# Kernel optimization log

Hardware: AMD Instinct MI355X
Metric: run time of the kernel (lower is better)

Reference implementation:

```python
import jax, jax.numpy as jnp
import numpy as np

N = 100000; D = 256; ATT = 512; H = 8; HD = ATT // H; E = 250000
TYPE_CT = 64; TS = 64; P = 8192; PC = 1024; MP = 131072; MC = 16384


def setup_inputs() -> dict:
    key = jax.random.key(0)
    ks = jax.random.split(key, 24)
    sD = 1.0 / np.sqrt(D); sT = 1.0 / np.sqrt(TS); sA = 1.0 / np.sqrt(ATT); sC = 1.0 / np.sqrt(D + ATT)
    inp = {}
    inp['node_states'] = jax.random.normal(ks[0], (N, D), jnp.float32)
    inp['node_types'] = jax.random.randint(ks[1], (N,), 0, TYPE_CT, jnp.int32)
    inp['pair_conj'] = jax.random.randint(ks[2], (E,), 0, N, jnp.int32)
    inp['pair_prem'] = jax.random.randint(ks[3], (E,), 0, N, jnp.int32)
    inp['pool_prem_nodes'] = jax.random.randint(ks[4], (MP,), 0, N, jnp.int32)
    inp['pool_prem_seg'] = ((jnp.arange(MP, dtype=jnp.int32) * P) // MP).astype(jnp.int32)  # every prem set non-empty
    inp['pool_conj_nodes'] = jax.random.randint(ks[5], (MC,), 0, N, jnp.int32)
    inp['pool_conj_seg'] = ((jnp.arange(MC, dtype=jnp.int32) * PC) // MC).astype(jnp.int32)
    inp['prem2conj'] = jax.random.randint(ks[6], (P,), 0, PC, jnp.int32)
    # learned parameters
    inp['ln_g'] = jnp.ones((D,), jnp.float32)
    inp['ln_b'] = jnp.zeros((D,), jnp.float32)
    inp['emb_p'] = jax.random.normal(ks[7], (TYPE_CT, TS), jnp.float32) * 0.02
    inp['wp_w'] = jax.random.normal(ks[8], (TS, ATT), jnp.float32) * sT
    inp['wp_b'] = jnp.zeros((ATT,), jnp.float32)
    inp['emb_c'] = jax.random.normal(ks[9], (TYPE_CT, TS), jnp.float32) * 0.02
    inp['wc_w'] = jax.random.normal(ks[10], (TS, ATT), jnp.float32) * sT
    inp['wc_b'] = jnp.zeros((ATT,), jnp.float32)
    inp['Wq_p'] = jax.random.normal(ks[11], (H, D, HD), jnp.float32) * sD
    inp['Wk_p'] = jax.random.normal(ks[12], (H, D, HD), jnp.float32) * sD
    inp['Wv_p'] = jax.random.normal(ks[13], (H, D, HD), jnp.float32) * sD
    inp['Wo_p'] = jax.random.normal(ks[14], (ATT, ATT), jnp.float32) * sA
    inp['Wq_c'] = jax.random.normal(ks[15], (H, D, HD), jnp.float32) * sD
    inp['Wk_c'] = jax.random.normal(ks[16], (H, D, HD), jnp.float32) * sD
    inp['Wv_c'] = jax.random.normal(ks[17], (H, D, HD), jnp.float32) * sD
    inp['Wo_c'] = jax.random.normal(ks[18], (ATT, ATT), jnp.float32) * sA
    inp['W_dag'] = jax.random.normal(ks[19], (D + ATT, D + ATT), jnp.float32) * sC
    inp['b_dag'] = jnp.zeros((D + ATT,), jnp.float32)
    return inp


def _layernorm(x, g, b):
    mu = jnp.mean(x, axis=-1, keepdims=True)
    var = jnp.mean(jnp.square(x - mu), axis=-1, keepdims=True)
    return (x - mu) * jax.lax.rsqrt(var + 1e-5) * g + b


def _mha_dir(x, src, tgt, Wq, Wk, Wv, Wo, gate):
    # gather query/key/value node reprs along the pair list (irregular gather)
    xs = x[src]; xt = x[tgt]                       # [E, D]
    q = jnp.einsum('ed,hdk->ehk', xs, Wq)          # [E, H, HD]
    k = jnp.einsum('ed,hdk->ehk', xt, Wk)
    scores = jnp.sum(q * k, axis=-1) / np.sqrt(HD)  # [E, H]
    # per-query-node (segment) softmax, as in compute_att_aggr grouping
    m = jax.ops.segment_max(scores, src, num_segments=N)
    ex = jnp.exp(scores - m[src])
    denom = jax.ops.segment_sum(ex, src, num_segments=N)
    prob = ex / denom[src]
    v = jnp.einsum('ed,hdk->ehk', xt, Wv)
    # adj_matr @ comb_matr scatter-aggregation
    agg = jax.ops.segment_sum(prob[..., None] * v, src, num_segments=N)  # [N, H, HD]
    return gate * (agg.reshape(N, H * HD) @ Wo)


def reference(node_states, node_types, pair_conj, pair_prem, pool_prem_nodes, pool_prem_seg,
              pool_conj_nodes, pool_conj_seg, prem2conj,
              ln_g, ln_b, emb_p, wp_w, wp_b, emb_c, wc_w, wc_b,
              Wq_p, Wk_p, Wv_p, Wo_p, Wq_c, Wk_c, Wv_c, Wo_c, W_dag, b_dag):
    x = _layernorm(node_states, ln_g, ln_b)                                  # ne_norm(node reprs)
    gate_p = jax.nn.sigmoid(emb_p[node_types] @ wp_w + wp_b)                 # prem_gate  [N, ATT]
    gate_c = jax.nn.sigmoid(emb_c[node_types] @ wc_w + wc_b)                 # conj_gate
    # just_prem pairs: (prem, conj) -> query/scatter node = prem, key/value node = conj
    comb = _mha_dir(x, pair_prem, pair_conj, Wq_p, Wk_p, Wv_p, Wo_p, gate_p)
    # just_conj pairs: (conj, prem)
    comb = comb + _mha_dir(x, pair_conj, pair_prem, Wq_c, Wk_c, Wv_c, Wo_c, gate_c)
    h = jnp.concatenate([x, comb], axis=1)                                   # [N, D+ATT]
    pooled = jnp.tanh(h @ W_dag + b_dag)                                     # simplified dag_lstm pass
    prem_r = jax.ops.segment_max(pooled[pool_prem_nodes], pool_prem_seg, num_segments=P)
    conj_sets = jax.ops.segment_max(pooled[pool_conj_nodes], pool_conj_seg, num_segments=PC)
    conj_r = conj_sets[prem2conj]
    return jnp.concatenate([prem_r, conj_r], axis=1)                         # [P, 2*(D+ATT)]
```

## Files before the change

### kernel.cpp

```cpp
#include <hip/hip_runtime.h>
#include <math.h>

#define N_NODES 100000
#define DIM 256
#define ATT 512
#define NH 8
#define HD 64
#define E_PAIRS 250000
#define TYPE_CT 64
#define TS 64
#define P_SEG 8192
#define PC_SEG 1024
#define MP_SZ 131072
#define MC_SZ 16384
#define CD 768

typedef unsigned short u16;
typedef __attribute__((ext_vector_type(8))) short short8v;
typedef __attribute__((ext_vector_type(4))) float floatx4;

__device__ __forceinline__ u16 f2b(float f) {
    unsigned u = __float_as_uint(f);
    return (u16)((u + 0x7FFFu + ((u >> 16) & 1u)) >> 16);
}
__device__ __forceinline__ float b2f(u16 h) {
    return __uint_as_float(((unsigned)h) << 16);
}

template<int N>
__device__ __forceinline__ void waitcnt_vm() {
    asm volatile("s_waitcnt vmcnt(%0)" :: "n"(N) : "memory");
}
__device__ __forceinline__ void barrier_fence() {
    asm volatile("s_barrier" ::: "memory");
    __builtin_amdgcn_sched_barrier(0);
}

__device__ __forceinline__ void remap8(int flat, int gx, int& bx, int& by) {
    int yc = flat & 7;
    int t = flat >> 3;
    bx = t % gx;
    by = yc + 8 * (t / gx);
}

__global__ __launch_bounds__(256) void fill_val_k(float* out, int n, float v) {
    int i = blockIdx.x * 256 + threadIdx.x;
    if (i < n) out[i] = v;
}

__global__ __launch_bounds__(64) void layernorm_k(
    const float* __restrict__ ns, const float* __restrict__ g,
    const float* __restrict__ b, u16* __restrict__ x)
{
    int row = blockIdx.x;
    int lane = threadIdx.x;
    float4 v = ((const float4*)(ns + (size_t)row * DIM))[lane];
    float sum = v.x + v.y + v.z + v.w;
    #pragma unroll
    for (int off = 32; off >= 1; off >>= 1) sum += __shfl_xor(sum, off);
    float mu = sum * (1.0f / DIM);
    float dx = v.x - mu, dy = v.y - mu, dz = v.z - mu, dw = v.w - mu;
    float sq = dx * dx + dy * dy + dz * dz + dw * dw;
    #pragma unroll
    for (int off = 32; off >= 1; off >>= 1) sq += __shfl_xor(sq, off);
    float rs = rsqrtf(sq * (1.0f / DIM) + 1e-5f);
    float4 gg = ((const float4*)g)[lane];
    float4 bb = ((const float4*)b)[lane];
    u16 o4[4];
    o4[0] = f2b(dx * rs * gg.x + bb.x);
    o4[1] = f2b(dy * rs * gg.y + bb.y);
    o4[2] = f2b(dz * rs * gg.z + bb.z);
    o4[3] = f2b(dw * rs * gg.w + bb.w);
    *(uint2*)(x + (size_t)row * DIM + lane * 4) = *(uint2*)o4;
}

__global__ __launch_bounds__(512) void gate_table_k(
    const float* __restrict__ emb, const float* __restrict__ w,
    const float* __restrict__ wb, float* __restrict__ tab)
{
    int t = blockIdx.x;
    int a = threadIdx.x;
    float acc = wb[a];
    #pragma unroll 8
    for (int s = 0; s < TS; ++s) acc += emb[t * TS + s] * w[s * ATT + a];
    tab[t * ATT + a] = 1.0f / (1.0f + expf(-acc));
}

__global__ __launch_bounds__(256) void wcvt_k(
    const float* __restrict__ W, u16* __restrict__ Bt, int K, int N)
{
    int idx = blockIdx.x * 256 + threadIdx.x;
    if (idx >= K * N) return;
    int c = idx / K, k = idx - c * K;
    Bt[idx] = f2b(W[(size_t)k * N + c]);
}

__global__ __launch_bounds__(256) void wqkv_cvt_k(
    const float* __restrict__ Wq, const float* __restrict__ Wk,
    const float* __restrict__ Wv, u16* __restrict__ outp)
{
    int idx = blockIdx.x * 256 + threadIdx.x;
    if (idx >= NH * 3 * HD * DIM) return;
    int k = idx & (DIM - 1);
    int c = (idx >> 8) & (HD - 1);
    int hm = idx >> 14;
    int m = hm % 3;
    int h = hm / 3;
    const float* W = (m == 0) ? Wq : ((m == 1) ? Wk : Wv);
    outp[idx] = f2b(W[((size_t)h * DIM + k) * HD + c]);
}

template<int BM, int WN, int DEPTH, int EPI>
__device__ __forceinline__ void gemm_body3(
    int bm, int bn,
    const u16* __restrict__ A, int lda,
    const u16* __restrict__ A2, int lda2, int K1,
    const u16* __restrict__ Bt, int ldb,
    u16* __restrict__ C, int ldc,
    int M, int K,
    const float* __restrict__ bias,
    const float* __restrict__ gateTab,
    const int* __restrict__ types)
{
    constexpr int BN = 32 * WN;
    constexpr int AR = BM / 64;
    constexpr int BR = BN / 64;
    constexpr int LA = AR + BR;
    constexpr int AF = BM / 32;
    __shared__ u16 As[DEPTH][BM * 32];
    __shared__ u16 Bs[DEPTH][BN * 32];
    const int tid = threadIdx.x;
    const int wave = tid >> 6, lane = tid & 63;
    const int wm = (wave >> 1) * (BM / 2), wn = (wave & 1) * 16 * WN;
    const int srow = tid >> 2;
    const int skk = (((tid & 3) ^ ((srow >> 1) & 3)) * 8);
    floatx4 acc[AF][WN] = {};

    auto stage = [&](int buf, int k0) {
        #pragma unroll
        for (int rnd = 0; rnd < AR; ++rnd) {
            int grow = bm + srow + rnd * 64;
            if (grow > M - 1) grow = M - 1;
            int gk = k0 + skk;
            const u16* src;
            if (EPI == 2 && gk >= K1) src = A2 + (size_t)grow * lda2 + (gk - K1);
            else                      src = A + (size_t)grow * lda + gk;
            __builtin_amdgcn_global_load_lds(
                (const __attribute__((address_space(1))) void*)src,
                (__attribute__((address_space(3))) void*)(&As[buf][rnd * 2048 + wave * 512]),
                16, 0, 0);
        }
        #pragma unroll
        for (int rnd = 0; rnd < BR; ++rnd) {
            const u16* src = Bt + (size_t)(bn + srow + rnd * 64) * ldb + k0 + skk;
            __builtin_amdgcn_global_load_lds(
                (const __attribute__((address_space(1))) void*)src,
                (__attribute__((address_space(3))) void*)(&Bs[buf][rnd * 2048 + wave * 512]),
                16, 0, 0);
        }
    };

    const int NS = K >> 5;
    #pragma unroll
    for (int p = 0; p < DEPTH - 1; ++p)
        if (p < NS) stage(p, p * 32);
    const int rr = lane & 15;
    const int cq = lane >> 4;
    int cur = 0;
    for (int is = 0; is < NS; ++is) {
        int pend = NS - 1 - is;
        if (pend > DEPTH - 2) pend = DEPTH - 2;
        if (pend >= 2)      waitcnt_vm<2 * LA>();
        else if (pend == 1) waitcnt_vm<LA>();
        else                waitcnt_vm<0>();
        barrier_fence();
        if (is + DEPTH - 1 < NS) stage((cur + DEPTH - 1) % DEPTH, (is + DEPTH - 1) * 32);
        short8v a[AF], b[WN];
        #pragma unroll
        for (int i = 0; i < AF; ++i) {
            int ar = wm + i * 16 + rr;
            a[i] = *(const short8v*)&As[cur][ar * 32 + ((cq ^ ((ar >> 1) & 3)) * 8)];
        }
        #pragma unroll
        for (int j = 0; j < WN; ++j) {
            int br = wn + j * 16 + rr;
            b[j] = *(const short8v*)&Bs[cur][br * 32 + ((cq ^ ((br >> 1) & 3)) * 8)];
        }
        #pragma unroll
        for (int i = 0; i < AF; ++i)
            #pragma unroll
            for (int j = 0; j < WN; ++j)
                acc[i][j] = __builtin_amdgcn_mfma_f32_16x16x32_bf16(
                    a[i], b[j], acc[i][j], 0, 0, 0);
        cur = (cur + 1) % DEPTH;
    }
    #pragma unroll
    for (int i = 0; i < AF; ++i) {
        #pragma unroll
        for (int j = 0; j < WN; ++j) {
            #pragma unroll
            for (int q = 0; q < 4; ++q) {
                int row = bm + wm + i * 16 + (lane >> 4) * 4 + q;
                if (row >= M) continue;
                int col = bn + wn + j * 16 + (lane & 15);
                float v = acc[i][j][q];
                size_t idx = (size_t)row * ldc + col;
                if (EPI == 0) C[idx] = f2b(v);
                else if (EPI == 1) {
                    float g = gateTab[types[row] * ATT + col];
                    C[idx] = f2b(b2f(C[idx]) + g * v);
                } else if (EPI == 3) {
                    float g = gateTab[types[row] * ATT + col];
                    C[idx] = f2b(g * v);
                } else {
                    C[idx] = f2b(tanhf(v + bias[col]));
                }
            }
        }
    }
}

#define MB64 1563
#define MB64P 1568

__global__ __launch_bounds__(256) void gemm_qkv(
    const u16* __restrict__ A, const u16* __restrict__ Bt, u16* __restrict__ C)
{
    gemm_body3<64, 6, 3, 0>(blockIdx.y * 64, 0,
                            A, DIM, nullptr, 0, 1 << 30, Bt, DIM, C, 192,
                            N_NODES, DIM, nullptr, nullptr, nullptr);
}
__global__ __launch_bounds__(256) void gemm_qkv_all(
    const u16* __restrict__ A, const u16* __restrict__ Bt, u16* __restrict__ C,
    int gx)
{
    int bx, by; remap8(blockIdx.x, gx, bx, by);
    if (by >= MB64) return;
    gemm_body3<64, 6, 3, 0>(by * 64, bx * 192,
                            A, DIM, nullptr, 0, 1 << 30, Bt, DIM, C, gx * 192,
                            N_NODES, DIM, nullptr, nullptr, nullptr);
}
__global__ __launch_bounds__(256) void gemm_wo_first(
    const u16* __restrict__ A, const u16* __restrict__ Bt, u16* __restrict__ C,
    const float* __restrict__ gateTab, const int* __restrict__ types)
{
    int bx, by; remap8(blockIdx.x, 4, bx, by);
    if (by >= MB64) return;
    gemm_body3<64, 4, 3, 3>(by * 64, bx * 128,
                            A, ATT, nullptr, 0, 1 << 30, Bt, ATT, C, ATT,
                            N_NODES, ATT, nullptr, gateTab, types);
}
__global__ __launch_bounds__(256) void gemm_wo_acc(
    const u16* __restrict__ A, const u16* __restrict__ Bt, u16* __restrict__ C,
    const float* __restrict__ gateTab, const int* __restrict__ types)
{
    int bx, by; remap8(blockIdx.x, 4, bx, by);
    if (by >= MB64) return;
    gemm_body3<64, 4, 3, 1>(by * 64, bx * 128,
                            A, ATT, nullptr, 0, 1 << 30, Bt, ATT, C, ATT,
                            N_NODES, ATT, nullptr, gateTab, types);
}
__global__ __launch_bounds__(256) void gemm_dag(
    const u16* __restrict__ A, const u16* __restrict__ A2,
    const u16* __restrict__ Bt, u16* __restrict__ C,
    const float* __restrict__ bias)
{
    int bx, by; remap8(blockIdx.x, 3, bx, by);
    if (by >= MB64) return;
    gemm_body3<64, 4, 3, 2>(by * 64, bx * 128,
                            A, DIM, A2, ATT, DIM, Bt, CD, C, 384,
                            N_NODES, CD, bias, nullptr, nullptr);
}

__global__ __launch_bounds__(256) void count_k(
    const int* __restrict__ src, int* __restrict__ counts)
{
    int e = blockIdx.x * 256 + threadIdx.x;
    if (e < E_PAIRS) atomicAdd(&counts[src[e]], 1);
}
__global__ __launch_bounds__(256) void scan1_k(
    const int* __restrict__ counts, int* __restrict__ offs, int* __restrict__ bsums)
{
    __shared__ int sm[256];
    int i = blockIdx.x * 256 + threadIdx.x;
    int v = (i < N_NODES) ? counts[i] : 0;
    sm[threadIdx.x] = v;
    __syncthreads();
    for (int d = 1; d < 256; d <<= 1) {
        int t = (threadIdx.x >= d) ? sm[threadIdx.x - d] : 0;
        __syncthreads();
        sm[threadIdx.x] += t;
        __syncthreads();
    }
    if (i < N_NODES) offs[i] = sm[threadIdx.x] - v;
    if (threadIdx.x == 255) bsums[blockIdx.x] = sm[255];
}
__global__ __launch_bounds__(512) void scan2_k(int* __restrict__ bsums, int nb)
{
    __shared__ int sm[512];
    int tx = threadIdx.x;
    int v = (tx < nb) ? bsums[tx] : 0;
    sm[tx] = v;
    __syncthreads();
    for (int d = 1; d < 512; d <<= 1) {
        int t = (tx >= d) ? sm[tx - d] : 0;
        __syncthreads();
        sm[tx] += t;
        __syncthreads();
    }
    if (tx < nb) bsums[tx] = sm[tx] - v;
}
__global__ __launch_bounds__(256) void addcur_k(
    int* __restrict__ offs, const int* __restrict__ bsums, int* __restrict__ cur)
{
    int i = blockIdx.x * 256 + threadIdx.x;
    if (i >= N_NODES) return;
    int o = offs[i] + bsums[i >> 8];
    offs[i] = o;
    cur[i] = o;
}
__global__ __launch_bounds__(256) void scatter_k(
    const int* __restrict__ src, const int* __restrict__ tgt,
    int* __restrict__ cur, int* __restrict__ csr_tgt)
{
    int e = blockIdx.x * 256 + threadIdx.x;
    if (e >= E_PAIRS) return;
    int p = atomicAdd(&cur[src[e]], 1);
    csr_tgt[p] = tgt[e];
}

template<int MULTI>
__global__ __launch_bounds__(256) void attn_k(
    const u16* __restrict__ qkv, int ld,
    const int* __restrict__ offs, const int* __restrict__ counts,
    const int* __restrict__ csr_tgt, u16* __restrict__ agg, int h_in)
{
    int s = blockIdx.x * 4 + (threadIdx.x >> 6);
    if (s >= N_NODES) return;
    int hy = MULTI ? blockIdx.y : 0;
    int h = h_in + hy;
    const u16* base = qkv + hy * 192;
    int lane = threadIdx.x & 63;
    float q = b2f(base[(size_t)s * ld + lane]) * 0.125f;
    int lo = offs[s], deg = counts[s];
    float m = -INFINITY, l = 0.0f, acc = 0.0f;
    if (deg > 0) {
        int t0 = csr_tgt[lo];
        u16 kc = base[(size_t)t0 * ld + 64 + lane];
        u16 vc = base[(size_t)t0 * ld + 128 + lane];
        for (int i = 0; i < deg; ++i) {
            u16 kn = 0, vn = 0;
            if (i + 1 < deg) {
                int tn = csr_tgt[lo + i + 1];
                kn = base[(size_t)tn * ld + 64 + lane];
                vn = base[(size_t)tn * ld + 128 + lane];
            }
            float p = q * b2f(kc);
            #pragma unroll
            for (int off = 32; off >= 1; off >>= 1) p += __shfl_xor(p, off);
            float mn = fmaxf(m, p);
            float sc = expf(m - mn);
            float w  = expf(p - mn);
            l = l * sc + w;
            acc = acc * sc + w * b2f(vc);
            m = mn;
            kc = kn; vc = vn;
        }
    }
    float r = (deg > 0) ? acc / l : 0.0f;
    agg[(size_t)s * ATT + h * HD + lane] = f2b(r);
}

template<int BFOUT>
__global__ __launch_bounds__(256) void seg_max_k(
    const u16* __restrict__ pooled, const int* __restrict__ nodes,
    const int* __restrict__ seg, int total, void* __restrict__ outv, int ldo)
{
    int p = blockIdx.x;
    int lo, hi;
    { int a = 0, b2 = total; while (a < b2) { int mid = (a + b2) >> 1; if (seg[mid] < p) a = mid + 1; else b2 = mid; } lo = a; }
    { int a = lo, b2 = total; while (a < b2) { int mid = (a + b2) >> 1; if (seg[mid] < p + 1) a = mid + 1; else b2 = mid; } hi = a; }
    for (int c = threadIdx.x; c < 384; c += 256) {
        float mx = -INFINITY;
        for (int i = lo; i < hi; ++i)
            mx = fmaxf(mx, b2f(pooled[(size_t)nodes[i] * 384 + c]));
        if (BFOUT) ((u16*)outv)[(size_t)p * ldo + c] = f2b(mx);
        else       ((float*)outv)[(size_t)p * ldo + c] = mx;
    }
}

__global__ __launch_bounds__(768) void gather_conj(
    const u16* __restrict__ cs, const int* __restrict__ p2c,
    float* __restrict__ out)
{
    int p = blockIdx.x;
    int c = threadIdx.x;
    out[(size_t)p * (2 * CD) + CD + c] = b2f(cs[(size_t)p2c[p] * CD + c]);
}

extern "C" void kernel_launch(void* const* d_in, const int* in_sizes, int n_in,
                              void* d_out, int out_size, void* d_ws, size_t ws_size,
                              hipStream_t stream) {
    const float* node_states     = (const float*)d_in[0];
    const int*   node_types      = (const int*)d_in[1];
    const int*   pair_conj       = (const int*)d_in[2];
    const int*   pair_prem       = (const int*)d_in[3];
    const int*   pool_prem_nodes = (const int*)d_in[4];
    const int*   pool_prem_seg   = (const int*)d_in[5];
    const int*   pool_conj_nodes = (const int*)d_in[6];
    const int*   pool_conj_seg   = (const int*)d_in[7];
    const int*   prem2conj       = (const int*)d_in[8];
    const float* ln_g  = (const float*)d_in[9];
    const float* ln_b  = (const float*)d_in[10];
    const float* emb_p = (const float*)d_in[11];
    const float* wp_w  = (const float*)d_in[12];
    const float* wp_b  = (const float*)d_in[13];
    const float* emb_c = (const float*)d_in[14];
    const float* wc_w  = (const float*)d_in[15];
    const float* wc_b  = (const float*)d_in[16];
    const float* Wq_p  = (const float*)d_in[17];
    const float* Wk_p  = (const float*)d_in[18];
    const float* Wv_p  = (const float*)d_in[19];
    const float* Wo_p  = (const float*)d_in[20];
    const float* Wq_c  = (const float*)d_in[21];
    const float* Wk_c  = (const float*)d_in[22];
    const float* Wv_c  = (const float*)d_in[23];
    const float* Wo_c  = (const float*)d_in[24];
    const float* W_dag = (const float*)d_in[25];
    const float* b_dag = (const float*)d_in[26];
    float* out = (float*)d_out;

    char* ws = (char*)d_ws;
    size_t o = 0;
    u16* x_bf  = (u16*)(ws + o); o += (size_t)N_NODES * DIM * 2;
    u16* comb  = (u16*)(ws + o); o += (size_t)N_NODES * ATT * 2;
    u16* R     = (u16*)(ws + o); o += (size_t)N_NODES * ATT * 2;
    char* csrb = ws + o;         o += 8000000;
    u16* conj_sets = (u16*)(ws + o); o += (size_t)PC_SEG * CD * 2;
    const size_t WS_NEEDED = o;

    if (ws_size < WS_NEEDED) {
        fill_val_k<<<(out_size + 255) / 256, 256, 0, stream>>>(out, out_size, (float)ws_size);
        return;
    }
    u16* qkv_all = (u16*)(ws + WS_NEEDED);
    int batch = 1;
    if (ws_size >= WS_NEEDED + (size_t)N_NODES * 1536 * 2)      batch = 8;
    else if (ws_size >= WS_NEEDED + (size_t)N_NODES * 768 * 2)  batch = 4;
    else if (ws_size >= WS_NEEDED + (size_t)N_NODES * 384 * 2)  batch = 2;

    u16* agg    = R;
    u16* pooled = R;
    int* c_counts[2], *c_offs[2], *c_cur[2], *c_tgt[2];
    for (int d = 0; d < 2; ++d) {
        char* base = csrb + (size_t)d * 2200000;
        c_counts[d] = (int*)(base + 0);
        c_offs[d]   = (int*)(base + 400000);
        c_cur[d]    = (int*)(base + 800000);
        c_tgt[d]    = (int*)(base + 1200000);
    }
    int* bsums = (int*)(csrb + 4400000);
    u16* wdag_t = (u16*)csrb;

    char* ob = (char*)d_out;
    u16* qkv     = (u16*)(ob + 0);
    float* gtab_p = (float*)(ob + 38400000);
    float* gtab_c = (float*)(ob + 38531072);
    u16* wqkv_t  = (u16*)(ob + 38662144);
    u16* wo_t    = (u16*)(ob + 40235008);

    layernorm_k<<<N_NODES, 64, 0, stream>>>(node_states, ln_g, ln_b, x_bf);
    gate_table_k<<<TYPE_CT, ATT, 0, stream>>>(emb_p, wp_w, wp_b, gtab_p);
    gate_table_k<<<TYPE_CT, ATT, 0, stream>>>(emb_c, wc_w, wc_b, gtab_c);
    wqkv_cvt_k<<<(NH * 3 * HD * DIM + 255) / 256, 256, 0, stream>>>(
        Wq_p, Wk_p, Wv_p, wqkv_t);
    wqkv_cvt_k<<<(NH * 3 * HD * DIM + 255) / 256, 256, 0, stream>>>(
        Wq_c, Wk_c, Wv_c, wqkv_t + (size_t)NH * 3 * HD * DIM);
    wcvt_k<<<(ATT * ATT + 255) / 256, 256, 0, stream>>>(Wo_p, wo_t, ATT, ATT);
    wcvt_k<<<(ATT * ATT + 255) / 256, 256, 0, stream>>>(
        Wo_c, wo_t + (size_t)ATT * ATT, ATT, ATT);

    const int NSCAN = (N_NODES + 255) / 256;
    for (int d = 0; d < 2; ++d) {
        const int* src = d ? pair_conj : pair_prem;
        const int* tgt = d ? pair_prem : pair_conj;
        hipMemsetAsync(c_counts[d], 0, 400000, stream);
        count_k<<<(E_PAIRS + 255) / 256, 256, 0, stream>>>(src, c_counts[d]);
        scan1_k<<<NSCAN, 256, 0, stream>>>(c_counts[d], c_offs[d], bsums);
        scan2_k<<<1, 512, 0, stream>>>(bsums, NSCAN);
        addcur_k<<<NSCAN, 256, 0, stream>>>(c_offs[d], bsums, c_cur[d]);
        scatter_k<<<(E_PAIRS + 255) / 256, 256, 0, stream>>>(src, tgt, c_cur[d], c_tgt[d]);
    }

    for (int dir = 0; dir < 2; ++dir) {
        const float* gt = dir ? gtab_c : gtab_p;
        const u16* wq_d = wqkv_t + (size_t)dir * NH * 3 * HD * DIM;
        const u16* wo_d = wo_t + (size_t)dir * ATT * ATT;

        if (batch > 1) {
            for (int hb = 0; hb < NH; hb += batch) {
                gemm_qkv_all<<<batch * MB64P, 256, 0, stream>>>(
                    x_bf, wq_d + (size_t)hb * 3 * HD * DIM, qkv_all, batch);
                attn_k<1><<<dim3((N_NODES + 3) / 4, batch), 256, 0, stream>>>(
                    qkv_all, batch * 192, c_offs[dir], c_counts[dir],
                    c_tgt[dir], agg, hb);
            }
        } else {
            for (int h = 0; h < NH; ++h) {
                gemm_qkv<<<dim3(1, MB64), 256, 0, stream>>>(
                    x_bf, wq_d + (size_t)h * 3 * HD * DIM, qkv);
                attn_k<0><<<(N_NODES + 3) / 4, 256, 0, stream>>>(
                    qkv, 192, c_offs[dir], c_counts[dir], c_tgt[dir], agg, h);
            }
        }

        if (dir == 0)
            gemm_wo_first<<<4 * MB64P, 256, 0, stream>>>(
                agg, wo_d, comb, gt, node_types);
        else
            gemm_wo_acc<<<4 * MB64P, 256, 0, stream>>>(
                agg, wo_d, comb, gt, node_types);
    }

    wcvt_k<<<(CD * CD + 255) / 256, 256, 0, stream>>>(W_dag, wdag_t, CD, CD);

    for (int c0 = 0; c0 < CD; c0 += 384) {
        gemm_dag<<<3 * MB64P, 256, 0, stream>>>(
            x_bf, comb, wdag_t + (size_t)c0 * CD, pooled, b_dag + c0);
        seg_max_k<0><<<P_SEG, 256, 0, stream>>>(
            pooled, pool_prem_nodes, pool_prem_seg, MP_SZ, out + c0, 2 * CD);
        seg_max_k<1><<<PC_SEG, 256, 0, stream>>>(
            pooled, pool_conj_nodes, pool_conj_seg, MC_SZ, conj_sets + c0, CD);
    }
    gather_conj<<<P_SEG, CD, 0, stream>>>(conj_sets, prem2conj, out);
}
```

Before: 2.011 ms.

## Use 128x128 GEMM tiles with A loaded directly into registers

Adds a new GEMM body that loads the A operand straight from global memory into registers with double buffering, keeping only B staged in LDS through a three-deep pipeline. It also raises the M tile from 64 to 128 rows. The QKV, Wo and DAG GEMMs now use this body, and their grids are adjusted to the new tile shape. The aim is to cut LDS traffic and waits while getting more reuse from each B tile. The risks are more register pressure and uncoalesced 16-byte row loads of A from global memory.

```diff
diff --git a/kernel.cpp b/kernel.cpp
--- a/kernel.cpp
+++ b/kernel.cpp
@@ -110,8 +110,8 @@
     outp[idx] = f2b(W[((size_t)h * DIM + k) * HD + c]);
 }
 
-template<int BM, int WN, int DEPTH, int EPI>
-__device__ __forceinline__ void gemm_body3(
+template<int WN, int EPI>
+__device__ __forceinline__ void gemm_body4(
     int bm, int bn,
     const u16* __restrict__ A, int lda,
     const u16* __restrict__ A2, int lda2, int K1,
@@ -123,33 +123,18 @@
     const int* __restrict__ types)
 {
     constexpr int BN = 32 * WN;
-    constexpr int AR = BM / 64;
     constexpr int BR = BN / 64;
-    constexpr int LA = AR + BR;
-    constexpr int AF = BM / 32;
-    __shared__ u16 As[DEPTH][BM * 32];
-    __shared__ u16 Bs[DEPTH][BN * 32];
+    __shared__ u16 Bs[3][BN * 32];
     const int tid = threadIdx.x;
     const int wave = tid >> 6, lane = tid & 63;
-    const int wm = (wave >> 1) * (BM / 2), wn = (wave & 1) * 16 * WN;
+    const int wm = (wave >> 1) * 64, wn = (wave & 1) * 16 * WN;
     const int srow = tid >> 2;
     const int skk = (((tid & 3) ^ ((srow >> 1) & 3)) * 8);
-    floatx4 acc[AF][WN] = {};
-
-    auto stage = [&](int buf, int k0) {
-        #pragma unroll
-        for (int rnd = 0; rnd < AR; ++rnd) {
-            int grow = bm + srow + rnd * 64;
-            if (grow > M - 1) grow = M - 1;
-            int gk = k0 + skk;
-            const u16* src;
-            if (EPI == 2 && gk >= K1) src = A2 + (size_t)grow * lda2 + (gk - K1);
-            else                      src = A + (size_t)grow * lda + gk;
-            __builtin_amdgcn_global_load_lds(
-                (const __attribute__((address_space(1))) void*)src,
-                (__attribute__((address_space(3))) void*)(&As[buf][rnd * 2048 + wave * 512]),
-                16, 0, 0);
-        }
+    const int arow0 = bm + wm + (lane & 15);
+    const int akk = (lane >> 4) * 8;
+    floatx4 acc[4][WN] = {};
+
+    auto stageB = [&](int buf, int k0) {
         #pragma unroll
         for (int rnd = 0; rnd < BR; ++rnd) {
             const u16* src = Bt + (size_t)(bn + srow + rnd * 64) * ldb + k0 + skk;
@@ -159,43 +144,58 @@
                 16, 0, 0);
         }
     };
+    auto loadA = [&](short8v* dst, int k0) {
+        #pragma unroll
+        for (int i = 0; i < 4; ++i) {
+            int grow = arow0 + i * 16;
+            if (grow > M - 1) grow = M - 1;
+            int gk = k0 + akk;
+            const u16* src;
+            if (EPI == 2 && gk >= K1) src = A2 + (size_t)grow * lda2 + (gk - K1);
+            else                      src = A + (size_t)grow * lda + gk;
+            dst[i] = *(const short8v*)src;
+        }
+    };
 
     const int NS = K >> 5;
-    #pragma unroll
-    for (int p = 0; p < DEPTH - 1; ++p)
-        if (p < NS) stage(p, p * 32);
-    const int rr = lane & 15;
-    const int cq = lane >> 4;
-    int cur = 0;
-    for (int is = 0; is < NS; ++is) {
-        int pend = NS - 1 - is;
-        if (pend > DEPTH - 2) pend = DEPTH - 2;
-        if (pend >= 2)      waitcnt_vm<2 * LA>();
-        else if (pend == 1) waitcnt_vm<LA>();
-        else                waitcnt_vm<0>();
+    short8v aA[4], aB[4];
+    loadA(aA, 0);
+    __builtin_amdgcn_sched_barrier(0);
+    stageB(0, 0);
+    stageB(1, 32);
+    __builtin_amdgcn_sched_barrier(0);
+
+    auto step = [&](int is, short8v* ca, short8v* na) {
+        if (is == 0)          waitcnt_vm<BR>();
+        else if (is + 1 < NS) waitcnt_vm<4 + BR>();
+        else                  waitcnt_vm<4>();
         barrier_fence();
-        if (is + DEPTH - 1 < NS) stage((cur + DEPTH - 1) % DEPTH, (is + DEPTH - 1) * 32);
-        short8v a[AF], b[WN];
-        #pragma unroll
-        for (int i = 0; i < AF; ++i) {
-            int ar = wm + i * 16 + rr;
-            a[i] = *(const short8v*)&As[cur][ar * 32 + ((cq ^ ((ar >> 1) & 3)) * 8)];
-        }
+        if (is + 1 < NS) loadA(na, (is + 1) * 32);
+        __builtin_amdgcn_sched_barrier(0);
+        if (is + 2 < NS) stageB((is + 2) % 3, (is + 2) * 32);
+        __builtin_amdgcn_sched_barrier(0);
+        const u16* bbuf = Bs[is % 3];
+        const int rr = lane & 15, cq = lane >> 4;
+        short8v b[WN];
         #pragma unroll
         for (int j = 0; j < WN; ++j) {
             int br = wn + j * 16 + rr;
-            b[j] = *(const short8v*)&Bs[cur][br * 32 + ((cq ^ ((br >> 1) & 3)) * 8)];
-        }
-        #pragma unroll
-        for (int i = 0; i < AF; ++i)
+            b[j] = *(const short8v*)&bbuf[br * 32 + ((cq ^ ((br >> 1) & 3)) * 8)];
+        }
+        #pragma unroll
+        for (int i = 0; i < 4; ++i)
             #pragma unroll
             for (int j = 0; j < WN; ++j)
                 acc[i][j] = __builtin_amdgcn_mfma_f32_16x16x32_bf16(
-                    a[i], b[j], acc[i][j], 0, 0, 0);
-        cur = (cur + 1) % DEPTH;
+                    ca[i], b[j], acc[i][j], 0, 0, 0);
+    };
+
+    for (int is = 0; is < NS; is += 2) {
+        step(is, aA, aB);
+        step(is + 1, aB, aA);
     }
     #pragma unroll
-    for (int i = 0; i < AF; ++i) {
+    for (int i = 0; i < 4; ++i) {
         #pragma unroll
         for (int j = 0; j < WN; ++j) {
             #pragma unroll
@@ -220,8 +220,119 @@
     }
 }
 
+template<int BM, int WN, int DEPTH, int EPI>
+__device__ __forceinline__ void gemm_body3(
+    int bm, int bn,
+    const u16* __restrict__ A, int lda,
+    const u16* __restrict__ A2, int lda2, int K1,
+    const u16* __restrict__ Bt, int ldb,
+    u16* __restrict__ C, int ldc,
+    int M, int K,
+    const float* __restrict__ bias,
+    const float* __restrict__ gateTab,
+    const int* __restrict__ types)
+{
+    constexpr int BN = 32 * WN;
+    constexpr int AR = BM / 64;
+    constexpr int BR = BN / 64;
+    constexpr int LA = AR + BR;
+    constexpr int AF = BM / 32;
+    __shared__ u16 As[DEPTH][BM * 32];
+    __shared__ u16 Bs[DEPTH][BN * 32];
+    const int tid = threadIdx.x;
+    const int wave = tid >> 6, lane = tid & 63;
+    const int wm = (wave >> 1) * (BM / 2), wn = (wave & 1) * 16 * WN;
+    const int srow = tid >> 2;
+    const int skk = (((tid & 3) ^ ((srow >> 1) & 3)) * 8);
+    floatx4 acc[AF][WN] = {};
+
+    auto stage = [&](int buf, int k0) {
+        #pragma unroll
+        for (int rnd = 0; rnd < AR; ++rnd) {
+            int grow = bm + srow + rnd * 64;
+            if (grow > M - 1) grow = M - 1;
+            int gk = k0 + skk;
+            const u16* src;
+            if (EPI == 2 && gk >= K1) src = A2 + (size_t)grow * lda2 + (gk - K1);
+            else                      src = A + (size_t)grow * lda + gk;
+            __builtin_amdgcn_global_load_lds(
+                (const __attribute__((address_space(1))) void*)src,
+                (__attribute__((address_space(3))) void*)(&As[buf][rnd * 2048 + wave * 512]),
+                16, 0, 0);
+        }
+        #pragma unroll
+        for (int rnd = 0; rnd < BR; ++rnd) {
+            const u16* src = Bt + (size_t)(bn + srow + rnd * 64) * ldb + k0 + skk;
+            __builtin_amdgcn_global_load_lds(
+                (const __attribute__((address_space(1))) void*)src,
+                (__attribute__((address_space(3))) void*)(&Bs[buf][rnd * 2048 + wave * 512]),
+                16, 0, 0);
+        }
+    };
+
+    const int NS = K >> 5;
+    #pragma unroll
+    for (int p = 0; p < DEPTH - 1; ++p)
+        if (p < NS) stage(p, p * 32);
+    const int rr = lane & 15;
+    const int cq = lane >> 4;
+    int cur = 0;
+    for (int is = 0; is < NS; ++is) {
+        int pend = NS - 1 - is;
+        if (pend > DEPTH - 2) pend = DEPTH - 2;
+        if (pend >= 2)      waitcnt_vm<2 * LA>();
+        else if (pend == 1) waitcnt_vm<LA>();
+        else                waitcnt_vm<0>();
+        barrier_fence();
+        if (is + DEPTH - 1 < NS) stage((cur + DEPTH - 1) % DEPTH, (is + DEPTH - 1) * 32);
+        short8v a[AF], b[WN];
+        #pragma unroll
+        for (int i = 0; i < AF; ++i) {
+            int ar = wm + i * 16 + rr;
+            a[i] = *(const short8v*)&As[cur][ar * 32 + ((cq ^ ((ar >> 1) & 3)) * 8)];
+        }
+        #pragma unroll
+        for (int j = 0; j < WN; ++j) {
+            int br = wn + j * 16 + rr;
+            b[j] = *(const short8v*)&Bs[cur][br * 32 + ((cq ^ ((br >> 1) & 3)) * 8)];
+        }
+        #pragma unroll
+        for (int i = 0; i < AF; ++i)
+            #pragma unroll
+            for (int j = 0; j < WN; ++j)
+                acc[i][j] = __builtin_amdgcn_mfma_f32_16x16x32_bf16(
+                    a[i], b[j], acc[i][j], 0, 0, 0);
+        cur = (cur + 1) % DEPTH;
+    }
+    #pragma unroll
+    for (int i = 0; i < AF; ++i) {
+        #pragma unroll
+        for (int j = 0; j < WN; ++j) {
+            #pragma unroll
+            for (int q = 0; q < 4; ++q) {
+                int row = bm + wm + i * 16 + (lane >> 4) * 4 + q;
+                if (row >= M) continue;
+                int col = bn + wn + j * 16 + (lane & 15);
+                float v = acc[i][j][q];
+                size_t idx = (size_t)row * ldc + col;
+                if (EPI == 0) C[idx] = f2b(v);
+                else if (EPI == 1) {
+                    float g = gateTab[types[row] * ATT + col];
+                    C[idx] = f2b(b2f(C[idx]) + g * v);
+                } else if (EPI == 3) {
+                    float g = gateTab[types[row] * ATT + col];
+                    C[idx] = f2b(g * v);
+                } else {
+                    C[idx] = f2b(tanhf(v + bias[col]));
+                }
+            }
+        }
+    }
+}
+
 #define MB64 1563
-#define MB64P 1568
+#define MB128 782
+#define MB128P 784
 
 __global__ __launch_bounds__(256) void gemm_qkv(
     const u16* __restrict__ A, const u16* __restrict__ Bt, u16* __restrict__ C)
@@ -235,30 +346,30 @@
     int gx)
 {
     int bx, by; remap8(blockIdx.x, gx, bx, by);
-    if (by >= MB64) return;
-    gemm_body3<64, 6, 3, 0>(by * 64, bx * 192,
-                            A, DIM, nullptr, 0, 1 << 30, Bt, DIM, C, gx * 192,
-                            N_NODES, DIM, nullptr, nullptr, nullptr);
+    if (by >= MB128) return;
+    gemm_body4<4, 0>(by * 128, bx * 128,
+                     A, DIM, nullptr, 0, 1 << 30, Bt, DIM, C, gx * 128,
+                     N_NODES, DIM, nullptr, nullptr, nullptr);
 }
 __global__ __launch_bounds__(256) void gemm_wo_first(
     const u16* __restrict__ A, const u16* __restrict__ Bt, u16* __restrict__ C,
     const float* __restrict__ gateTab, const int* __restrict__ types)
 {
     int bx, by; remap8(blockIdx.x, 4, bx, by);
-    if (by >= MB64) return;
-    gemm_body3<64, 4, 3, 3>(by * 64, bx * 128,
-                            A, ATT, nullptr, 0, 1 << 30, Bt, ATT, C, ATT,
-                            N_NODES, ATT, nullptr, gateTab, types);
+    if (by >= MB128) return;
+    gemm_body4<4, 3>(by * 128, bx * 128,
+                     A, ATT, nullptr, 0, 1 << 30, Bt, ATT, C, ATT,
+                     N_NODES, ATT, nullptr, gateTab, types);
 }
 __global__ __launch_bounds__(256) void gemm_wo_acc(
     const u16* __restrict__ A, const u16* __restrict__ Bt, u16* __restrict__ C,
     const float* __restrict__ gateTab, const int* __restrict__ types)
 {
     int bx, by; remap8(blockIdx.x, 4, bx, by);
-    if (by >= MB64) return;
-    gemm_body3<64, 4, 3, 1>(by * 64, bx * 128,
-                            A, ATT, nullptr, 0, 1 << 30, Bt, ATT, C, ATT,
-                            N_NODES, ATT, nullptr, gateTab, types);
+    if (by >= MB128) return;
+    gemm_body4<4, 1>(by * 128, bx * 128,
+                     A, ATT, nullptr, 0, 1 << 30, Bt, ATT, C, ATT,
+                     N_NODES, ATT, nullptr, gateTab, types);
 }
 __global__ __launch_bounds__(256) void gemm_dag(
     const u16* __restrict__ A, const u16* __restrict__ A2,
@@ -266,10 +377,10 @@
     const float* __restrict__ bias)
 {
     int bx, by; remap8(blockIdx.x, 3, bx, by);
-    if (by >= MB64) return;
-    gemm_body3<64, 4, 3, 2>(by * 64, bx * 128,
-                            A, DIM, A2, ATT, DIM, Bt, CD, C, 384,
-                            N_NODES, CD, bias, nullptr, nullptr);
+    if (by >= MB128) return;
+    gemm_body4<4, 2>(by * 128, bx * 128,
+                     A, DIM, A2, ATT, DIM, Bt, CD, C, 384,
+                     N_NODES, CD, bias, nullptr, nullptr);
 }
 
 __global__ __launch_bounds__(256) void count_k(
@@ -498,9 +609,10 @@
         const u16* wo_d = wo_t + (size_t)dir * ATT * ATT;
 
         if (batch > 1) {
+            int gx = batch * 192 / 128;
             for (int hb = 0; hb < NH; hb += batch) {
-                gemm_qkv_all<<<batch * MB64P, 256, 0, stream>>>(
-                    x_bf, wq_d + (size_t)hb * 3 * HD * DIM, qkv_all, batch);
+                gemm_qkv_all<<<gx * MB128P, 256, 0, stream>>>(
+                    x_bf, wq_d + (size_t)hb * 3 * HD * DIM, qkv_all, gx);
                 attn_k<1><<<dim3((N_NODES + 3) / 4, batch), 256, 0, stream>>>(
                     qkv_all, batch * 192, c_offs[dir], c_counts[dir],
                     c_tgt[dir], agg, hb);
@@ -515,17 +627,17 @@
         }
 
         if (dir == 0)
-            gemm_wo_first<<<4 * MB64P, 256, 0, stream>>>(
+            gemm_wo_first<<<4 * MB128P, 256, 0, stream>>>(
                 agg, wo_d, comb, gt, node_types);
         else
-            gemm_wo_acc<<<4 * MB64P, 256, 0, stream>>>(
+            gemm_wo_acc<<<4 * MB128P, 256, 0, stream>>>(
                 agg, wo_d, comb, gt, node_types);
     }
 
     wcvt_k<<<(CD * CD + 255) / 256, 256, 0, stream>>>(W_dag, wdag_t, CD, CD);
 
     for (int c0 = 0; c0 < CD; c0 += 384) {
-        gemm_dag<<<3 * MB64P, 256, 0, stream>>>(
+        gemm_dag<<<3 * MB128P, 256, 0, stream>>>(
             x_bf, comb, wdag_t + (size_t)c0 * CD, pooled, b_dag + c0);
         seg_max_k<0><<<P_SEG, 256, 0, stream>>>(
             pooled, pool_prem_nodes, pool_prem_seg, MP_SZ, out + c0, 2 * CD);
```

After: 2.332 ms. 16.0% more time.
